# Kernel tuning notes

Measured on AMD Instinct MI355X. Metric: run time of the kernel, lower is better.

The kernel has to match this reference:

```python
import jax, jax.numpy as jnp
import numpy as np


def setup_inputs() -> dict:
    key = jax.random.key(0)
    k1, k2, k3 = jax.random.split(key, 3)
    B, C, H, W = 32, 768, 24, 24
    feat1 = jax.random.normal(k1, (B, C, H, W), dtype=jnp.float32)
    feat2 = jax.random.normal(k2, (B, C, H, W), dtype=jnp.float32)
    gamma = jax.random.normal(k3, (1,), dtype=jnp.float32)
    return {"feat1": feat1, "feat2": feat2, "gamma": gamma}


def reference(feat1, feat2, gamma):
    # CMA: channel-wise cross-modal attention over flattened spatial dim.
    B, C, H, W = feat1.shape
    q = feat1.reshape(B, C, H * W)          # [B, C, HW]
    kv = feat2.reshape(B, C, H * W)         # [B, C, HW] (k and v share this)
    attn = jnp.einsum('bcn,bdn->bcd', q, kv)          # [B, C, C] = q @ k^T
    attn = jax.nn.softmax(attn, axis=-1)
    info = jnp.einsum('bcd,bdn->bcn', attn, kv)       # [B, C, HW]
    info = info.reshape(B, C, H, W)
    return gamma[0] * info + feat1
```

## Files before the change

### kernel.cpp

```cpp
#include <hip/hip_runtime.h>

#define B_  32
#define C_  768
#define HW_ 576

#define NCQ 18
#define NCP 24

typedef _Float16 half8 __attribute__((ext_vector_type(8)));
typedef _Float16 half4 __attribute__((ext_vector_type(4)));
typedef float    f32x4 __attribute__((ext_vector_type(4)));

__device__ __forceinline__ void g2l16(const void* g, void* l) {
    __builtin_amdgcn_global_load_lds(
        (const __attribute__((address_space(1))) unsigned int*)g,
        (__attribute__((address_space(3))) unsigned int*)l, 16, 0, 0);
}

__device__ __forceinline__ int xcd_swz(int orig, int nwg) {
    int q = nwg >> 3, rr = nwg & 7;
    int xcd = orig & 7, idx = orig >> 3;
    int base = (xcd < rr) ? xcd * (q + 1) : rr * (q + 1) + (xcd - rr) * q;
    return base + idx;
}

#define VM(N) asm volatile("s_waitcnt vmcnt(" #N ")" ::: "memory")

__global__ __launch_bounds__(256) void prep_all(const float* __restrict__ f1,
                                                const float* __restrict__ f2,
                                                char* __restrict__ q16,
                                                char* __restrict__ kv16,
                                                char* __restrict__ vt,
                                                int b0, int nqk) {
    __shared__ float Vsh[32 * 201];
    const int bid = blockIdx.x;
    if (bid < nqk) {
        int idx = bid * 256 + threadIdx.x;
        int x   = idx & 3;
        int row = (idx >> 2) & 127;
        int t3  = idx >> 9;
        int k0  = t3 % 18;
        int t4  = t3 / 18;
        int ti  = t4 % 6;
        int bz  = t4 / 6;
        int kc  = x ^ ((row >> 1) & 3);
        size_t src = ((size_t)(b0 + bz) * C_ + ti * 128 + row) * HW_ + k0 * 32 + kc * 8;
        f32x4 a0 = *(const f32x4*)(f1 + src);
        f32x4 a1 = *(const f32x4*)(f1 + src + 4);
        f32x4 c0 = *(const f32x4*)(f2 + src);
        f32x4 c1 = *(const f32x4*)(f2 + src + 4);
        half8 ha, hb;
        #pragma unroll
        for (int e = 0; e < 4; ++e) {
            ha[e] = (_Float16)a0[e]; ha[4 + e] = (_Float16)a1[e];
            hb[e] = (_Float16)c0[e]; hb[4 + e] = (_Float16)c1[e];
        }
        *(half8*)(q16  + (size_t)idx * 16) = ha;
        *(half8*)(kv16 + (size_t)idx * 16) = hb;
    } else {
        int bid2 = bid - nqk;
        int bz = bid2 / 72, rem = bid2 % 72, k0 = rem / 3, tj = rem % 3;
        int b  = b0 + bz;
        int t  = threadIdx.x;
        #pragma unroll
        for (int p = 0; p < 6; ++p) {
            int fidx = p * 256 + t;
            int dd = fidx / 48, c4 = fidx % 48;
            f32x4 v = *(const f32x4*)(f2 + ((size_t)b * C_ + k0 * 32 + dd) * HW_ + tj * 192 + c4 * 4);
            #pragma unroll
            for (int e = 0; e < 4; ++e) Vsh[dd * 201 + c4 * 4 + e] = v[e];
        }
        __syncthreads();
        char* ob = vt + ((size_t)(bz * 3 + tj) * NCP + k0) * 12288;
        #pragma unroll
        for (int p = 0; p < 3; ++p) {
            int o = p * 256 + t;
            int x = o & 3, n = o >> 2;
            int kc = x ^ ((n >> 1) & 3);
            half8 h;
            #pragma unroll
            for (int j = 0; j < 8; ++j) h[j] = (_Float16)Vsh[(kc * 8 + j) * 201 + n];
            *(half8*)(ob + o * 16) = h;
        }
    }
}

__global__ __launch_bounds__(512, 4) void qk6(const char* __restrict__ q16,
                                              const char* __restrict__ kv16,
                                              float* __restrict__ attn,
                                              int nwg) {
    __shared__ __align__(16) char S[3][24576];
    const int wg = xcd_swz(blockIdx.x, nwg);
    const int bz = wg >> 4, rr0 = wg & 15, ti = rr0 >> 2, tj = rr0 & 3;
    const int t = threadIdx.x, lane = t & 63, w = t >> 6;
    const int rsub = lane >> 2, cb = (lane & 3) * 16;

    const char *p0, *p1, *p2;
    int o0, o1, o2;
    {
        auto arow = [&](int l) {
            int gr = ti * 192 + 16 * l + rsub;
            return q16 + ((size_t)(bz * 6 + (gr >> 7)) * NCQ) * 8192 + (gr & 127) * 64 + cb;
        };
        auto brow = [&](int l) {
            int gd = tj * 192 + 16 * l + rsub;
            return kv16 + ((size_t)(bz * 6 + (gd >> 7)) * NCQ) * 8192 + (gd & 127) * 64 + cb;
        };
        if (w < 4) {
            p0 = arow(2 * w);     o0 = (2 * w) * 1024;
            p1 = arow(2 * w + 1); o1 = (2 * w + 1) * 1024;
            p2 = brow(8 + w);     o2 = 12288 + (8 + w) * 1024;
        } else {
            int v = w - 4;
            p0 = brow(2 * v);     o0 = 12288 + (2 * v) * 1024;
            p1 = brow(2 * v + 1); o1 = 12288 + (2 * v + 1) * 1024;
            p2 = arow(8 + v);     o2 = (8 + v) * 1024;
        }
    }

    const int wr = (w >> 1) * 48, wc = (w & 1) * 96;
    const int r16 = lane & 15, cg = lane >> 4;
    int offA[3], offB[6];
    #pragma unroll
    for (int m = 0; m < 3; ++m) {
        int ra = wr + m * 16 + r16;
        offA[m] = ra * 64 + ((cg ^ ((ra >> 1) & 3)) << 4);
    }
    #pragma unroll
    for (int n = 0; n < 6; ++n) {
        int rb = wc + n * 16 + r16;
        offB[n] = 12288 + rb * 64 + ((cg ^ ((rb >> 1) & 3)) << 4);
    }

    f32x4 acc[3][6] = {};

#define STG(SLOT) do {                          \
        char* sb_ = &S[SLOT][0];                \
        g2l16(p0, sb_ + o0);                    \
        g2l16(p1, sb_ + o1);                    \
        g2l16(p2, sb_ + o2);                    \
        p0 += 8192; p1 += 8192; p2 += 8192;     \
    } while (0)

    STG(0); STG(1);
    int rd = 0, st = 2;
    for (int c = 0; c < NCQ; ++c) {
        if (c + 2 < NCQ) {
            STG(st); st = (st == 2) ? 0 : st + 1;
            VM(6);
        } else if (c + 2 == NCQ) {
            VM(3);
        } else {
            VM(0);
        }
        __builtin_amdgcn_s_barrier();
        const char* sb = &S[rd][0];
        rd = (rd == 2) ? 0 : rd + 1;
        half8 a0 = *(const half8*)(sb + offA[0]);
        half8 a1 = *(const half8*)(sb + offA[1]);
        half8 a2 = *(const half8*)(sb + offA[2]);
        __builtin_amdgcn_s_setprio(1);
        #pragma unroll
        for (int n = 0; n < 6; ++n) {
            half8 bn = *(const half8*)(sb + offB[n]);
            acc[0][n] = __builtin_amdgcn_mfma_f32_16x16x32_f16(a0, bn, acc[0][n], 0, 0, 0);
            acc[1][n] = __builtin_amdgcn_mfma_f32_16x16x32_f16(a1, bn, acc[1][n], 0, 0, 0);
            acc[2][n] = __builtin_amdgcn_mfma_f32_16x16x32_f16(a2, bn, acc[2][n], 0, 0, 0);
        }
        __builtin_amdgcn_s_setprio(0);
        __builtin_amdgcn_s_barrier();
    }
#undef STG

    float* ab = attn + ((size_t)bz * C_ + ti * 192) * C_ + tj * 192;
    const int col = lane & 15, rbase = (lane >> 4) * 4;
    #pragma unroll
    for (int m = 0; m < 3; ++m)
        #pragma unroll
        for (int n = 0; n < 6; ++n)
            #pragma unroll
            for (int rg = 0; rg < 4; ++rg)
                ab[(size_t)(wr + m * 16 + rbase + rg) * C_ + wc + n * 16 + col] = acc[m][n][rg];
}

__global__ __launch_bounds__(256) void sm_stats(const float* __restrict__ attn,
                                                float* __restrict__ stats,
                                                const float* __restrict__ gamma) {
    const int R    = blockIdx.x * 4 + (threadIdx.x >> 6);
    const int lane = threadIdx.x & 63;
    const float* p = attn + (size_t)R * C_;

    f32x4 v[3];
    float mx = -1e30f;
    #pragma unroll
    for (int u = 0; u < 3; ++u) {
        v[u] = *(const f32x4*)(p + (size_t)(lane + 64 * u) * 4);
        #pragma unroll
        for (int e = 0; e < 4; ++e) mx = fmaxf(mx, v[u][e]);
    }
    #pragma unroll
    for (int o = 32; o > 0; o >>= 1) mx = fmaxf(mx, __shfl_xor(mx, o));

    float s = 0.f;
    #pragma unroll
    for (int u = 0; u < 3; ++u)
        #pragma unroll
        for (int e = 0; e < 4; ++e) {
            s += __expf(v[u][e] - mx);
        }
    #pragma unroll
    for (int o = 32; o > 0; o >>= 1) s += __shfl_xor(s, o);

    if (lane == 0) {
        ((float2*)stats)[R] = make_float2(mx, gamma[0] / s);
    }
}

__global__ __launch_bounds__(512, 4) void pv8(const float* __restrict__ attn,
                                              const char* __restrict__ vt,
                                              const float* __restrict__ stats,
                                              const float* __restrict__ f1,
                                              float* __restrict__ out,
                                              int b0, int nwg) {
    __shared__ __align__(16) char S[3][20480];
    const int wg = xcd_swz(blockIdx.x, nwg);
    const int bz = wg / 18, rem = wg % 18, ti = rem / 3, tj = rem % 3;
    const int t = threadIdx.x, lane = t & 63, w = t >> 6;
    const int rsub = lane >> 2, cbb = (lane & 3) * 16;

    const int r0 = t >> 3;
    const int r1 = 64 + r0;
    const int d4 = t & 7;
    const float* srcA0 = attn + ((size_t)bz * C_ + ti * 128 + r0) * C_ + d4 * 4;
    const float* srcA1 = attn + ((size_t)bz * C_ + ti * 128 + r1) * C_ + d4 * 4;
    const float2 ms0 = ((const float2*)stats)[bz * C_ + ti * 128 + r0];
    const float2 ms1 = ((const float2*)stats)[bz * C_ + ti * 128 + r1];
    const int aw0 = r0 * 64 + (((d4 >> 1) ^ ((r0 >> 1) & 3)) << 4) + (d4 & 1) * 8;
    const int aw1 = r1 * 64 + (((d4 >> 1) ^ ((r1 >> 1) & 3)) << 4) + (d4 & 1) * 8;

    const char* vbase = vt + ((size_t)(bz * 3 + tj) * NCP) * 12288;
    const char *pB0, *pB1;
    int ob0, ob1;
    if (w < 4) {
        pB0 = vbase + (32 * w + rsub) * 64 + cbb;          ob0 = 8192 + (32 * w) * 64;
        pB1 = vbase + (32 * w + 16 + rsub) * 64 + cbb;     ob1 = 8192 + (32 * w + 16) * 64;
    } else {
        pB0 = vbase + (128 + 16 * (w - 4) + rsub) * 64 + cbb;
        ob0 = 8192 + (128 + 16 * (w - 4)) * 64;
        pB1 = vbase; ob1 = 0;
    }

    const int wr = (w >> 2) * 64, wc = (w & 3) * 48;
    const int r16 = lane & 15, cg = lane >> 4;
    int offA[4], offB[3];
    #pragma unroll
    for (int m = 0; m < 4; ++m) {
        int ra = wr + m * 16 + r16;
        offA[m] = ra * 64 + ((cg ^ ((ra >> 1) & 3)) << 4);
    }
    #pragma unroll
    for (int n = 0; n < 3; ++n) {
        int rb = wc + n * 16 + r16;
        offB[n] = 8192 + rb * 64 + ((cg ^ ((rb >> 1) & 3)) << 4);
    }

    f32x4 acc[4][3] = {};
    f32x4 va0, va1;

#define STG_B(SLOT) do {                                  \
        g2l16(pB0, &S[SLOT][0] + ob0); pB0 += 12288;      \
        if (w < 4) { g2l16(pB1, &S[SLOT][0] + ob1); pB1 += 12288; } \
    } while (0)
#define LD_A() do { va0 = *(const f32x4*)srcA0; va1 = *(const f32x4*)srcA1; \
                    srcA0 += 32; srcA1 += 32; } while (0)
#define WR_A(SLOT) do {                                                \
        half4 h0, h1;                                                  \
        _Pragma("unroll")                                              \
        for (int e = 0; e < 4; ++e) {                                  \
            h0[e] = (_Float16)(__expf(va0[e] - ms0.x) * ms0.y);        \
            h1[e] = (_Float16)(__expf(va1[e] - ms1.x) * ms1.y);        \
        }                                                              \
        *(half4*)(&S[SLOT][0] + aw0) = h0;                             \
        *(half4*)(&S[SLOT][0] + aw1) = h1;                             \
    } while (0)

    LD_A();
    WR_A(0);
    STG_B(0); STG_B(1);
    LD_A();

    for (int c = 0; c < NCP; ++c) {
        const int cur = c % 3;
        asm volatile("s_waitcnt lgkmcnt(0)" ::: "memory");
        __builtin_amdgcn_s_barrier();
        if (c + 2 < NCP) STG_B((c + 2) % 3);
        if (c < NCP - 2)      { if (w < 4) VM(6); else VM(4); }
        else if (c == NCP - 2){ if (w < 4) VM(4); else VM(3); }
        else                  { VM(0); }
        __builtin_amdgcn_s_barrier();

        const char* sb = &S[cur][0];
        half8 a[4], bb8[3];
        #pragma unroll
        for (int m = 0; m < 4; ++m) a[m]  = *(const half8*)(sb + offA[m]);
        #pragma unroll
        for (int n = 0; n < 3; ++n) bb8[n] = *(const half8*)(sb + offB[n]);
        __builtin_amdgcn_s_setprio(1);
        #pragma unroll
        for (int m = 0; m < 4; ++m)
            #pragma unroll
            for (int n = 0; n < 3; ++n)
                acc[m][n] = __builtin_amdgcn_mfma_f32_16x16x32_f16(a[m], bb8[n], acc[m][n], 0, 0, 0);
        __builtin_amdgcn_s_setprio(0);

        if (c + 1 < NCP) {
            WR_A((c + 1) % 3);
            if (c + 2 < NCP) LD_A();
        }
    }
#undef STG_B
#undef LD_A
#undef WR_A

    const int b = b0 + bz;
    const float* f1b = f1 + ((size_t)b * C_ + ti * 128) * HW_ + tj * 192;
    float*       ob  = out + ((size_t)b * C_ + ti * 128) * HW_ + tj * 192;
    const int col = lane & 15, rbase = (lane >> 4) * 4;
    #pragma unroll
    for (int m = 0; m < 4; ++m)
        #pragma unroll
        for (int n = 0; n < 3; ++n)
            #pragma unroll
            for (int rg = 0; rg < 4; ++rg) {
                int r2 = wr + m * 16 + rbase + rg;
                int c2 = wc + n * 16 + col;
                ob[(size_t)r2 * HW_ + c2] = acc[m][n][rg] + f1b[(size_t)r2 * HW_ + c2];
            }
}

extern "C" void kernel_launch(void* const* d_in, const int* in_sizes, int n_in,
                              void* d_out, int out_size, void* d_ws, size_t ws_size,
                              hipStream_t stream) {
    const float* feat1 = (const float*)d_in[0];
    const float* feat2 = (const float*)d_in[1];
    const float* gamma = (const float*)d_in[2];
    float* out = (float*)d_out;

    const size_t SZ_Q    = (size_t)C_ * HW_ * 2;
    const size_t SZ_ATTN = (size_t)C_ * C_  * 4;
    const size_t SZ_ST   = (size_t)C_ * 8;
    const size_t per_batch = SZ_ATTN + 3 * SZ_Q + SZ_ST;

    int nb = (int)(ws_size / per_batch);
    if (nb < 1) nb = 1;
    if (nb > B_) nb = B_;

    char* ws    = (char*)d_ws;
    float* attn = (float*)ws;
    char* q16   = ws + (size_t)nb * SZ_ATTN;
    char* kv16  = q16 + (size_t)nb * SZ_Q;
    char* vtb   = kv16 + (size_t)nb * SZ_Q;
    float* stats = (float*)(vtb + (size_t)nb * SZ_Q);

    for (int b0 = 0; b0 < B_; b0 += nb) {
        int cur = (B_ - b0 < nb) ? (B_ - b0) : nb;
        prep_all<<<cur * 288, 256, 0, stream>>>(feat1, feat2, q16, kv16, vtb, b0, cur * 216);
        qk6<<<cur * 16, 512, 0, stream>>>(q16, kv16, attn, cur * 16);
        sm_stats<<<cur * 192, 256, 0, stream>>>(attn, stats, gamma);
        pv8<<<cur * 18, 512, 0, stream>>>(attn, vtb, stats, feat1, out, b0, cur * 18);
    }
}
```

Measured before the change: 146.7 us.

## Fuse softmax row stats into QK epilogue and interleave batches across blocks

Result: faster. 143.1 us (-2.4%).

```diff
diff --git a/kernel.cpp b/kernel.cpp
--- a/kernel.cpp
+++ b/kernel.cpp
@@ -17,32 +17,25 @@
         (__attribute__((address_space(3))) unsigned int*)l, 16, 0, 0);
 }
 
-__device__ __forceinline__ int xcd_swz(int orig, int nwg) {
-    int q = nwg >> 3, rr = nwg & 7;
-    int xcd = orig & 7, idx = orig >> 3;
-    int base = (xcd < rr) ? xcd * (q + 1) : rr * (q + 1) + (xcd - rr) * q;
-    return base + idx;
-}
-
 #define VM(N) asm volatile("s_waitcnt vmcnt(" #N ")" ::: "memory")
+
 
 __global__ __launch_bounds__(256) void prep_all(const float* __restrict__ f1,
                                                 const float* __restrict__ f2,
                                                 char* __restrict__ q16,
                                                 char* __restrict__ kv16,
                                                 char* __restrict__ vt,
-                                                int b0, int nqk) {
+                                                int b0, int cur, int nqk) {
     __shared__ float Vsh[32 * 201];
     const int bid = blockIdx.x;
     if (bid < nqk) {
-        int idx = bid * 256 + threadIdx.x;
-        int x   = idx & 3;
-        int row = (idx >> 2) & 127;
-        int t3  = idx >> 9;
+        const int bz = bid % cur, u = bid / cur;
+        int g   = u * 256 + threadIdx.x;
+        int x   = g & 3;
+        int row = (g >> 2) & 127;
+        int t3  = g >> 9;
         int k0  = t3 % 18;
-        int t4  = t3 / 18;
-        int ti  = t4 % 6;
-        int bz  = t4 / 6;
+        int ti  = t3 / 18;
         int kc  = x ^ ((row >> 1) & 3);
         size_t src = ((size_t)(b0 + bz) * C_ + ti * 128 + row) * HW_ + k0 * 32 + kc * 8;
         f32x4 a0 = *(const f32x4*)(f1 + src);
@@ -55,11 +48,13 @@
             ha[e] = (_Float16)a0[e]; ha[4 + e] = (_Float16)a1[e];
             hb[e] = (_Float16)c0[e]; hb[4 + e] = (_Float16)c1[e];
         }
-        *(half8*)(q16  + (size_t)idx * 16) = ha;
-        *(half8*)(kv16 + (size_t)idx * 16) = hb;
+        size_t dst = ((size_t)(((size_t)bz * 6 + ti) * 18 + k0) << 9) | (g & 511);
+        *(half8*)(q16  + dst * 16) = ha;
+        *(half8*)(kv16 + dst * 16) = hb;
     } else {
         int bid2 = bid - nqk;
-        int bz = bid2 / 72, rem = bid2 % 72, k0 = rem / 3, tj = rem % 3;
+        const int bz = bid2 % cur, u = bid2 / cur;
+        int k0 = u / 3, tj = u % 3;
         int b  = b0 + bz;
         int t  = threadIdx.x;
         #pragma unroll
@@ -88,10 +83,12 @@
 __global__ __launch_bounds__(512, 4) void qk6(const char* __restrict__ q16,
                                               const char* __restrict__ kv16,
                                               float* __restrict__ attn,
-                                              int nwg) {
+                                              float2* __restrict__ part,
+                                              int cur) {
     __shared__ __align__(16) char S[3][24576];
-    const int wg = xcd_swz(blockIdx.x, nwg);
-    const int bz = wg >> 4, rr0 = wg & 15, ti = rr0 >> 2, tj = rr0 & 3;
+    const int wg = blockIdx.x;
+    const int bz = wg % cur, u = wg / cur;
+    const int ti = u >> 2, tj = u & 3;
     const int t = threadIdx.x, lane = t & 63, w = t >> 6;
     const int rsub = lane >> 2, cb = (lane & 3) * 16;
 
@@ -181,50 +178,59 @@
             #pragma unroll
             for (int rg = 0; rg < 4; ++rg)
                 ab[(size_t)(wr + m * 16 + rbase + rg) * C_ + wc + n * 16 + col] = acc[m][n][rg];
-}
-
-__global__ __launch_bounds__(256) void sm_stats(const float* __restrict__ attn,
-                                                float* __restrict__ stats,
-                                                const float* __restrict__ gamma) {
-    const int R    = blockIdx.x * 4 + (threadIdx.x >> 6);
-    const int lane = threadIdx.x & 63;
-    const float* p = attn + (size_t)R * C_;
-
-    f32x4 v[3];
-    float mx = -1e30f;
-    #pragma unroll
-    for (int u = 0; u < 3; ++u) {
-        v[u] = *(const f32x4*)(p + (size_t)(lane + 64 * u) * 4);
-        #pragma unroll
-        for (int e = 0; e < 4; ++e) mx = fmaxf(mx, v[u][e]);
-    }
-    #pragma unroll
-    for (int o = 32; o > 0; o >>= 1) mx = fmaxf(mx, __shfl_xor(mx, o));
-
+
+    const int half = w & 1;
+    #pragma unroll
+    for (int m = 0; m < 3; ++m)
+        #pragma unroll
+        for (int rg = 0; rg < 4; ++rg) {
+            float mx = -1e30f;
+            #pragma unroll
+            for (int n = 0; n < 6; ++n) mx = fmaxf(mx, acc[m][n][rg]);
+            #pragma unroll
+            for (int o = 1; o < 16; o <<= 1) mx = fmaxf(mx, __shfl_xor(mx, o));
+            float s = 0.f;
+            #pragma unroll
+            for (int n = 0; n < 6; ++n) s += __expf(acc[m][n][rg] - mx);
+            #pragma unroll
+            for (int o = 1; o < 16; o <<= 1) s += __shfl_xor(s, o);
+            if ((lane & 15) == 0) {
+                int row = wr + m * 16 + (lane >> 4) * 4 + rg;
+                part[((size_t)bz * C_ + ti * 192 + row) * 8 + tj * 2 + half] =
+                    make_float2(mx, s);
+            }
+        }
+}
+
+__global__ __launch_bounds__(256) void sm_combine(const float2* __restrict__ part,
+                                                  float2* __restrict__ stats,
+                                                  const float* __restrict__ gamma,
+                                                  int cur) {
+    const int bid = blockIdx.x;
+    const int bz = bid % cur, u = bid / cur;
+    const int R = bz * C_ + u * 256 + threadIdx.x;
+    float2 p[8];
+    #pragma unroll
+    for (int i = 0; i < 8; ++i) p[i] = part[(size_t)R * 8 + i];
+    float m = p[0].x;
+    #pragma unroll
+    for (int i = 1; i < 8; ++i) m = fmaxf(m, p[i].x);
     float s = 0.f;
     #pragma unroll
-    for (int u = 0; u < 3; ++u)
-        #pragma unroll
-        for (int e = 0; e < 4; ++e) {
-            s += __expf(v[u][e] - mx);
-        }
-    #pragma unroll
-    for (int o = 32; o > 0; o >>= 1) s += __shfl_xor(s, o);
-
-    if (lane == 0) {
-        ((float2*)stats)[R] = make_float2(mx, gamma[0] / s);
-    }
+    for (int i = 0; i < 8; ++i) s += p[i].y * __expf(p[i].x - m);
+    stats[R] = make_float2(m, gamma[0] / s);
 }
 
 __global__ __launch_bounds__(512, 4) void pv8(const float* __restrict__ attn,
                                               const char* __restrict__ vt,
-                                              const float* __restrict__ stats,
+                                              const float2* __restrict__ stats,
                                               const float* __restrict__ f1,
                                               float* __restrict__ out,
-                                              int b0, int nwg) {
+                                              int b0, int cur) {
     __shared__ __align__(16) char S[3][20480];
-    const int wg = xcd_swz(blockIdx.x, nwg);
-    const int bz = wg / 18, rem = wg % 18, ti = rem / 3, tj = rem % 3;
+    const int wg = blockIdx.x;
+    const int bz = wg % cur, u = wg / cur;
+    const int ti = u / 3, tj = u % 3;
     const int t = threadIdx.x, lane = t & 63, w = t >> 6;
     const int rsub = lane >> 2, cbb = (lane & 3) * 16;
 
@@ -233,8 +239,8 @@
     const int d4 = t & 7;
     const float* srcA0 = attn + ((size_t)bz * C_ + ti * 128 + r0) * C_ + d4 * 4;
     const float* srcA1 = attn + ((size_t)bz * C_ + ti * 128 + r1) * C_ + d4 * 4;
-    const float2 ms0 = ((const float2*)stats)[bz * C_ + ti * 128 + r0];
-    const float2 ms1 = ((const float2*)stats)[bz * C_ + ti * 128 + r1];
+    const float2 ms0 = stats[bz * C_ + ti * 128 + r0];
+    const float2 ms1 = stats[bz * C_ + ti * 128 + r1];
     const int aw0 = r0 * 64 + (((d4 >> 1) ^ ((r0 >> 1) & 3)) << 4) + (d4 & 1) * 8;
     const int aw1 = r1 * 64 + (((d4 >> 1) ^ ((r1 >> 1) & 3)) << 4) + (d4 & 1) * 8;
 
@@ -290,7 +296,7 @@
     LD_A();
 
     for (int c = 0; c < NCP; ++c) {
-        const int cur = c % 3;
+        const int cur3 = c % 3;
         asm volatile("s_waitcnt lgkmcnt(0)" ::: "memory");
         __builtin_amdgcn_s_barrier();
         if (c + 2 < NCP) STG_B((c + 2) % 3);
@@ -299,7 +305,7 @@
         else                  { VM(0); }
         __builtin_amdgcn_s_barrier();
 
-        const char* sb = &S[cur][0];
+        const char* sb = &S[cur3][0];
         half8 a[4], bb8[3];
         #pragma unroll
         for (int m = 0; m < 4; ++m) a[m]  = *(const half8*)(sb + offA[m]);
@@ -348,25 +354,27 @@
 
     const size_t SZ_Q    = (size_t)C_ * HW_ * 2;
     const size_t SZ_ATTN = (size_t)C_ * C_  * 4;
+    const size_t SZ_PART = (size_t)C_ * 8 * 8;
     const size_t SZ_ST   = (size_t)C_ * 8;
-    const size_t per_batch = SZ_ATTN + 3 * SZ_Q + SZ_ST;
+    const size_t per_batch = SZ_ATTN + 3 * SZ_Q + SZ_PART + SZ_ST;
 
     int nb = (int)(ws_size / per_batch);
     if (nb < 1) nb = 1;
     if (nb > B_) nb = B_;
 
-    char* ws    = (char*)d_ws;
-    float* attn = (float*)ws;
-    char* q16   = ws + (size_t)nb * SZ_ATTN;
-    char* kv16  = q16 + (size_t)nb * SZ_Q;
-    char* vtb   = kv16 + (size_t)nb * SZ_Q;
-    float* stats = (float*)(vtb + (size_t)nb * SZ_Q);
+    char* ws     = (char*)d_ws;
+    float* attn  = (float*)ws;
+    char* q16    = ws + (size_t)nb * SZ_ATTN;
+    char* kv16   = q16 + (size_t)nb * SZ_Q;
+    char* vtb    = kv16 + (size_t)nb * SZ_Q;
+    float2* part = (float2*)(vtb + (size_t)nb * SZ_Q);
+    float2* stats = (float2*)((char*)part + (size_t)nb * SZ_PART);
 
     for (int b0 = 0; b0 < B_; b0 += nb) {
         int cur = (B_ - b0 < nb) ? (B_ - b0) : nb;
-        prep_all<<<cur * 288, 256, 0, stream>>>(feat1, feat2, q16, kv16, vtb, b0, cur * 216);
-        qk6<<<cur * 16, 512, 0, stream>>>(q16, kv16, attn, cur * 16);
-        sm_stats<<<cur * 192, 256, 0, stream>>>(attn, stats, gamma);
-        pv8<<<cur * 18, 512, 0, stream>>>(attn, vtb, stats, feat1, out, b0, cur * 18);
-    }
-}
+        prep_all<<<cur * 288, 256, 0, stream>>>(feat1, feat2, q16, kv16, vtb, b0, cur, cur * 216);
+        qk6<<<cur * 16, 512, 0, stream>>>(q16, kv16, attn, part, cur);
+        sm_combine<<<cur * 3, 256, 0, stream>>>(part, stats, gamma, cur);
+        pv8<<<cur * 18, 512, 0, stream>>>(attn, vtb, stats, feat1, out, b0, cur);
+    }
+}
```
